# Kernel optimization log

Measured on AMD Instinct MI355X. Metric: run time of the kernel, lower is better.

Reference implementation:

```python
import jax, jax.numpy as jnp
import numpy as np

MAX_DISP = 4  # max_displacement; window = (2*MAX_DISP+1)**2 = 81 displacements


def setup_inputs() -> dict:
    key = jax.random.key(0)
    k1, k2 = jax.random.split(key)
    B, C, H, W = 8, 128, 128, 128
    in1 = jax.random.normal(k1, (B, C, H, W), dtype=jnp.float32)
    in2 = jax.random.normal(k2, (B, C, H, W), dtype=jnp.float32)
    return {"in1": in1, "in2": in2}


def reference(in1, in2):
    # Cost-volume correlation (kernel_size=1): for each displacement (dy,dx) in
    # [-d, d]^2, corr[b, w, y, x] = mean_c in1[b,c,y,x] * in2_pad[b,c,y+dy,x+dx],
    # matching torch unfold ordering: w = dy_idx*(2d+1) + dx_idx (row-major).
    B, C, H, W = in1.shape
    d = MAX_DISP
    in2_pad = jnp.pad(in2, ((0, 0), (0, 0), (d, d), (d, d)))  # zero pad, like ConstantPad2d
    corr = [
        jnp.mean(in1 * jax.lax.slice(in2_pad, (0, 0, dy, dx), (B, C, dy + H, dx + W)), axis=1)
        for dy in range(2 * d + 1)
        for dx in range(2 * d + 1)
    ]
    return jnp.stack(corr, axis=1)  # [B, (2d+1)^2, H, W]
```

## Files before the change

kernel.cpp:

```cpp
#include <hip/hip_runtime.h>


#define MAXD 4
#define ND 9
#define NDISP 81
#define BATCH 8
#define CH 128
#define HH 128
#define WW 128
#define HW (HH * WW)
#define CC 4
#define NCHUNK (CH / CC)
#define TY 4
#define NROW (TY + 2 * MAXD)
#define PITCH 132
#define CPC (NROW * PITCH)
#define CHF (CC * CPC)
#define CHFP 6400
#define NSLOT 25
#define NT 576

typedef const __attribute__((address_space(1))) float GAS;
typedef __attribute__((address_space(3))) float LAS;

__device__ __forceinline__ void dma16(const float* g, float* l) {
    __builtin_amdgcn_global_load_lds((GAS*)g, (LAS*)l, 16, 0, 0);
}
__device__ __forceinline__ float dpp_shr1(float x) {
    return __int_as_float(__builtin_amdgcn_update_dpp(
        0, __float_as_int(x), 0x111, 0xF, 0xF, true));
}
__device__ __forceinline__ float dpp_shl1(float x) {
    return __int_as_float(__builtin_amdgcn_update_dpp(
        0, __float_as_int(x), 0x101, 0xF, 0xF, true));
}

__global__ __launch_bounds__(NT, 1) void corr_kernel(
    const float* __restrict__ in1,
    const float* __restrict__ in2,
    float* __restrict__ out)
{
    __shared__ float s2[2][CHFP];

    const int tid = threadIdx.x;
    const int b   = blockIdx.x;
    const int y0  = blockIdx.y * TY;

    const int xg   = tid & 15;
    const int dy   = (tid >> 4) % ND;
    const int ly   = tid / (ND * 16);
    const int lane = tid & 63;
    const int rl   = ly + dy;
    const bool rok = (unsigned)(y0 + rl - MAXD) < (unsigned)HH;

    const float* in2b = in2 + (size_t)b * CH * HW;

    const int wv = __builtin_amdgcn_readfirstlane(tid >> 6);
    const float* gsrc[3];
    int lds_off[3];
    bool use[3];
    #pragma unroll
    for (int it = 0; it < 3; ++it) {
        int s   = wv + it * 9;
        use[it] = (s < NSLOT);
        int ss  = use[it] ? s : 0;
        int F   = ss * 256 + lane * 4;
        int c   = F / CPC;
        int f   = F - c * CPC;
        int R   = f / PITCH;
        int j   = f - R * PITCH;
        bool v  = (c < CC) && (j < WW);
        int rr  = y0 - MAXD + R;
        int srow = rr < 0 ? 0 : (rr >= HH ? HH - 1 : rr);
        gsrc[it]   = in2b + (v ? ((size_t)c * HW + (size_t)srow * WW + j) : 0);
        lds_off[it] = ss * 256;
    }

    float acc[ND][8];
    #pragma unroll
    for (int d = 0; d < ND; ++d)
        #pragma unroll
        for (int i = 0; i < 8; ++i) acc[d][i] = 0.0f;

    const float* ap = in1 + (size_t)b * CH * HW + (size_t)(y0 + ly) * WW + xg * 8;

    #pragma unroll
    for (int it = 0; it < 3; ++it)
        if (use[it]) dma16(gsrc[it], &s2[0][lds_off[it]]);
    #pragma unroll
    for (int it = 0; it < 3; ++it) gsrc[it] += CC * HW;
    __syncthreads();

    #pragma unroll 1
    for (int k = 0; k < NCHUNK; ++k) {
        const int p = k & 1;

        if (k + 1 < NCHUNK) {
            #pragma unroll
            for (int it = 0; it < 3; ++it)
                if (use[it]) dma16(gsrc[it], &s2[1 - p][lds_off[it]]);
            #pragma unroll
            for (int it = 0; it < 3; ++it) gsrc[it] += CC * HW;
        }

        #pragma unroll
        for (int cc = 0; cc < CC; ++cc) {
            const float* sp = &s2[p][cc * CPC + rl * PITCH + xg * 8];
            float4 wlo = *(const float4*)(sp);
            float4 whi = *(const float4*)(sp + 4);
            float w[8] = {wlo.x, wlo.y, wlo.z, wlo.w,
                          whi.x, whi.y, whi.z, whi.w};

            float W[16];
            W[0]  = dpp_shr1(w[4]);
            W[1]  = dpp_shr1(w[5]);
            W[2]  = dpp_shr1(w[6]);
            W[3]  = dpp_shr1(w[7]);
            #pragma unroll
            for (int i = 0; i < 8; ++i) W[4 + i] = w[i];
            W[12] = dpp_shl1(w[0]);
            W[13] = dpp_shl1(w[1]);
            W[14] = dpp_shl1(w[2]);
            W[15] = dpp_shl1(w[3]);

            const float* p1 = ap + (size_t)cc * HW;
            float4 a0 = *(const float4*)(p1);
            float4 a1 = *(const float4*)(p1 + 4);
            float a[8] = {a0.x, a0.y, a0.z, a0.w, a1.x, a1.y, a1.z, a1.w};

            #pragma unroll
            for (int d = 0; d < ND; ++d)
                #pragma unroll
                for (int i = 0; i < 8; ++i)
                    acc[d][i] = fmaf(a[i], W[i + d], acc[d][i]);
        }
        ap += CC * HW;
        __syncthreads();
    }

    const float sc = rok ? (1.0f / (float)CH) : 0.0f;
    float* outb = out + (size_t)b * NDISP * HW + (size_t)(y0 + ly) * WW + xg * 8;
    #pragma unroll
    for (int d = 0; d < ND; ++d) {
        float* op = outb + (size_t)(dy * ND + d) * HW;
        float4 v0 = make_float4(acc[d][0] * sc, acc[d][1] * sc,
                                acc[d][2] * sc, acc[d][3] * sc);
        float4 v1 = make_float4(acc[d][4] * sc, acc[d][5] * sc,
                                acc[d][6] * sc, acc[d][7] * sc);
        *(float4*)(op)     = v0;
        *(float4*)(op + 4) = v1;
    }
}

extern "C" void kernel_launch(void* const* d_in, const int* in_sizes, int n_in,
                              void* d_out, int out_size, void* d_ws, size_t ws_size,
                              hipStream_t stream) {
    const float* in1 = (const float*)d_in[0];
    const float* in2 = (const float*)d_in[1];
    float* out = (float*)d_out;
    dim3 grid(BATCH, HH / TY);
    corr_kernel<<<grid, NT, 0, stream>>>(in1, in2, out);
}
```

Measured before the change: 220.5 us.

## Halve row tile, stage in1 through LDS DMA, and run two blocks per CU

Row tile shrinks from 4 to 2 so each block has 320 threads (288 doing compute), and launch bounds now allow two blocks per CU. The in1 tile for each channel chunk is brought into LDS with the same async global_load_lds double buffer as in2, so in1 is no longer read directly from global memory in the inner loop. The aim is more latency hiding through occupancy and overlapped in1 loads. The cost is that each in2 row window is loaded for fewer output rows, so the halo overhead grows (10 rows loaded per 2 output rows instead of 12 per 4). The extra 32 threads per block sit idle during compute.

```diff
diff --git a/kernel.cpp b/kernel.cpp
--- a/kernel.cpp
+++ b/kernel.cpp
@@ -11,14 +11,16 @@
 #define HW (HH * WW)
 #define CC 4
 #define NCHUNK (CH / CC)
-#define TY 4
+#define TY 2
 #define NROW (TY + 2 * MAXD)
 #define PITCH 132
 #define CPC (NROW * PITCH)
-#define CHF (CC * CPC)
-#define CHFP 6400
+#define IN2SLOTS 21
+#define IN1OFF (IN2SLOTS * 256)
 #define NSLOT 25
-#define NT 576
+#define CHFP (NSLOT * 256)
+#define NT 320
+#define NACT 288
 
 typedef const __attribute__((address_space(1))) float GAS;
 typedef __attribute__((address_space(3))) float LAS;
@@ -35,7 +37,7 @@
         0, __float_as_int(x), 0x101, 0xF, 0xF, true));
 }
 
-__global__ __launch_bounds__(NT, 1) void corr_kernel(
+__global__ __launch_bounds__(NT, 2) void corr_kernel(
     const float* __restrict__ in1,
     const float* __restrict__ in2,
     float* __restrict__ out)
@@ -46,34 +48,39 @@
     const int b   = blockIdx.x;
     const int y0  = blockIdx.y * TY;
 
+    const bool act = tid < NACT;
     const int xg   = tid & 15;
     const int dy   = (tid >> 4) % ND;
-    const int ly   = tid / (ND * 16);
+    const int ly   = act ? (tid / 144) : 0;
     const int lane = tid & 63;
     const int rl   = ly + dy;
     const bool rok = (unsigned)(y0 + rl - MAXD) < (unsigned)HH;
 
+    const float* in1b = in1 + (size_t)b * CH * HW;
     const float* in2b = in2 + (size_t)b * CH * HW;
 
     const int wv = __builtin_amdgcn_readfirstlane(tid >> 6);
-    const float* gsrc[3];
-    int lds_off[3];
-    bool use[3];
+    const float* gsrc[5];
     #pragma unroll
-    for (int it = 0; it < 3; ++it) {
-        int s   = wv + it * 9;
-        use[it] = (s < NSLOT);
-        int ss  = use[it] ? s : 0;
-        int F   = ss * 256 + lane * 4;
-        int c   = F / CPC;
-        int f   = F - c * CPC;
-        int R   = f / PITCH;
-        int j   = f - R * PITCH;
-        bool v  = (c < CC) && (j < WW);
-        int rr  = y0 - MAXD + R;
-        int srow = rr < 0 ? 0 : (rr >= HH ? HH - 1 : rr);
-        gsrc[it]   = in2b + (v ? ((size_t)c * HW + (size_t)srow * WW + j) : 0);
-        lds_off[it] = ss * 256;
+    for (int it = 0; it < 5; ++it) {
+        int s = wv + it * 5;
+        if (s < IN2SLOTS) {
+            int F = s * 256 + lane * 4;
+            int c = F / CPC;
+            int f = F - c * CPC;
+            int R = f / PITCH;
+            int j = f - R * PITCH;
+            bool v = (c < CC) && (j < WW);
+            int rr = y0 - MAXD + R;
+            int sr = rr < 0 ? 0 : (rr >= HH ? HH - 1 : rr);
+            gsrc[it] = in2b + (v ? ((size_t)c * HW + (size_t)sr * WW + j) : 0);
+        } else {
+            int F   = (s - IN2SLOTS) * 256 + lane * 4;
+            int ly_ = F >> 9;
+            int c   = (F >> 7) & 3;
+            int x   = F & 127;
+            gsrc[it] = in1b + (size_t)c * HW + (size_t)(y0 + ly_) * WW + x;
+        }
     }
 
     float acc[ND][8];
@@ -82,13 +89,11 @@
         #pragma unroll
         for (int i = 0; i < 8; ++i) acc[d][i] = 0.0f;
 
-    const float* ap = in1 + (size_t)b * CH * HW + (size_t)(y0 + ly) * WW + xg * 8;
-
     #pragma unroll
-    for (int it = 0; it < 3; ++it)
-        if (use[it]) dma16(gsrc[it], &s2[0][lds_off[it]]);
+    for (int it = 0; it < 5; ++it)
+        dma16(gsrc[it], &s2[0][(wv + it * 5) * 256]);
     #pragma unroll
-    for (int it = 0; it < 3; ++it) gsrc[it] += CC * HW;
+    for (int it = 0; it < 5; ++it) gsrc[it] += CC * HW;
     __syncthreads();
 
     #pragma unroll 1
@@ -97,10 +102,10 @@
 
         if (k + 1 < NCHUNK) {
             #pragma unroll
-            for (int it = 0; it < 3; ++it)
-                if (use[it]) dma16(gsrc[it], &s2[1 - p][lds_off[it]]);
+            for (int it = 0; it < 5; ++it)
+                dma16(gsrc[it], &s2[1 - p][(wv + it * 5) * 256]);
             #pragma unroll
-            for (int it = 0; it < 3; ++it) gsrc[it] += CC * HW;
+            for (int it = 0; it < 5; ++it) gsrc[it] += CC * HW;
         }
 
         #pragma unroll
@@ -123,9 +128,9 @@
             W[14] = dpp_shl1(w[2]);
             W[15] = dpp_shl1(w[3]);
 
-            const float* p1 = ap + (size_t)cc * HW;
-            float4 a0 = *(const float4*)(p1);
-            float4 a1 = *(const float4*)(p1 + 4);
+            const float* apx = &s2[p][IN1OFF + (ly * CC + cc) * 128 + xg * 8];
+            float4 a0 = *(const float4*)(apx);
+            float4 a1 = *(const float4*)(apx + 4);
             float a[8] = {a0.x, a0.y, a0.z, a0.w, a1.x, a1.y, a1.z, a1.w};
 
             #pragma unroll
@@ -134,21 +139,23 @@
                 for (int i = 0; i < 8; ++i)
                     acc[d][i] = fmaf(a[i], W[i + d], acc[d][i]);
         }
-        ap += CC * HW;
         __syncthreads();
     }
 
-    const float sc = rok ? (1.0f / (float)CH) : 0.0f;
-    float* outb = out + (size_t)b * NDISP * HW + (size_t)(y0 + ly) * WW + xg * 8;
-    #pragma unroll
-    for (int d = 0; d < ND; ++d) {
-        float* op = outb + (size_t)(dy * ND + d) * HW;
-        float4 v0 = make_float4(acc[d][0] * sc, acc[d][1] * sc,
-                                acc[d][2] * sc, acc[d][3] * sc);
-        float4 v1 = make_float4(acc[d][4] * sc, acc[d][5] * sc,
-                                acc[d][6] * sc, acc[d][7] * sc);
-        *(float4*)(op)     = v0;
-        *(float4*)(op + 4) = v1;
+    if (act) {
+        const float sc = rok ? (1.0f / (float)CH) : 0.0f;
+        float* outb = out + (size_t)b * NDISP * HW
+                          + (size_t)(y0 + ly) * WW + xg * 8;
+        #pragma unroll
+        for (int d = 0; d < ND; ++d) {
+            float* op = outb + (size_t)(dy * ND + d) * HW;
+            float4 v0 = make_float4(acc[d][0] * sc, acc[d][1] * sc,
+                                    acc[d][2] * sc, acc[d][3] * sc);
+            float4 v1 = make_float4(acc[d][4] * sc, acc[d][5] * sc,
+                                    acc[d][6] * sc, acc[d][7] * sc);
+            *(float4*)(op)     = v0;
+            *(float4*)(op + 4) = v1;
+        }
     }
 }
 
```

Result: slower. 229.9 us (+4.3%).
